# Performance work log

Hardware: AMD Instinct MI355X
Metric: run time of the kernel (lower is better)

## Reference

```python
import jax, jax.numpy as jnp
import numpy as np

DIM = 1024
HEADS = 16
HEAD_DIM = DIM // HEADS
WINDOW = 128


def setup_inputs() -> dict:
    key = jax.random.key(0)
    k1, k2, k3, k4 = jax.random.split(key, 4)
    B, T = 2, 2048
    x = jax.random.normal(k1, (B, T, DIM), dtype=jnp.float32)
    # nn.Linear(dim, 3*dim, bias=False): weight [3*dim, dim]; y = x @ W.T
    W_qkv = jax.random.normal(k2, (3 * DIM, DIM), dtype=jnp.float32) * (1.0 / np.sqrt(DIM))
    W_proj = jax.random.normal(k3, (DIM, DIM), dtype=jnp.float32) * (1.0 / np.sqrt(DIM))
    b_proj = jax.random.normal(k4, (DIM,), dtype=jnp.float32) * 0.01
    return {"x": x, "W_qkv": W_qkv, "W_proj": W_proj, "b_proj": b_proj}


def reference(x, W_qkv, W_proj, b_proj) -> jnp.ndarray:
    B, T, C = x.shape
    scale = HEAD_DIM ** -0.5
    qkv = jnp.einsum('btc,oc->bto', x, W_qkv)  # [B,T,3*D]
    qkv = qkv.reshape(B, T, 3, HEADS, HEAD_DIM)
    qkv = jnp.transpose(qkv, (2, 0, 3, 1, 4))  # [3,B,H,T,hd]
    q, k, v = qkv[0], qkv[1], qkv[2]
    # sliding-window mask: attend iff |i-j| <= WINDOW
    idx = jnp.arange(T)
    mask = jnp.abs(idx[:, None] - idx[None, :]) <= WINDOW  # [T,T]
    scores = jnp.einsum('bhqd,bhkd->bhqk', q, k) * scale  # [B,H,T,T]
    scores = jnp.where(mask[None, None], scores, jnp.finfo(scores.dtype).min)
    attn = jax.nn.softmax(scores, axis=-1)
    out = jnp.einsum('bhqk,bhkd->bhqd', attn, v)  # [B,H,T,hd]
    out = jnp.transpose(out, (0, 2, 1, 3)).reshape(B, T, C)
    return jnp.einsum('btc,oc->bto', out, W_proj) + b_proj
```

## Files before the change

### kernel.cpp

```cpp
#include <hip/hip_runtime.h>
#include <hip/hip_bf16.h>
#include <cstdint>
#include <cstddef>

#define DIMC 1024
#define HEADS 16
#define HD 64
#define WINDOW 128
#define BB 2
#define TT 2048
#define NTOK (BB*TT)
#define QKVN (3*DIMC)

typedef __bf16 bf16;
typedef __bf16 bf16x8 __attribute__((ext_vector_type(8)));
typedef __bf16 bf16x4 __attribute__((ext_vector_type(4)));
typedef float f32x4 __attribute__((ext_vector_type(4)));
typedef unsigned int u32;

typedef const __attribute__((address_space(1))) u32* gp1_t;
typedef __attribute__((address_space(3))) u32* lp3_t;

__device__ __forceinline__ void gload16(const void* g, void* l) {
  __builtin_amdgcn_global_load_lds((gp1_t)g, (lp3_t)l, 16, 0, 0);
}

__device__ __forceinline__ u32 lds_u32(const void* p) {
  return (u32)(uintptr_t)(__attribute__((address_space(3))) const void*)p;
}

__device__ __forceinline__ void BAR() {
  asm volatile("" ::: "memory");
  __builtin_amdgcn_s_barrier();
  asm volatile("" ::: "memory");
}

__global__ void cast3_kernel(const float* __restrict__ x,
                             const float* __restrict__ wq,
                             const float* __restrict__ wp,
                             bf16* __restrict__ xo,
                             bf16* __restrict__ wqo,
                             bf16* __restrict__ wpo) {
  const int NX = NTOK * DIMC / 4;
  const int NQ = QKVN * DIMC / 4;
  const int NP = DIMC * DIMC / 4;
  const int total = NX + NQ + NP;
  typedef float float4v __attribute__((ext_vector_type(4)));
  for (int i = blockIdx.x * blockDim.x + threadIdx.x; i < total;
       i += gridDim.x * blockDim.x) {
    const float4v* src; bf16* dst; int j;
    if (i < NX)            { src = (const float4v*)x;  dst = xo;  j = i; }
    else if (i < NX + NQ)  { src = (const float4v*)wq; dst = wqo; j = i - NX; }
    else                   { src = (const float4v*)wp; dst = wpo; j = i - NX - NQ; }
    float4v v = src[j];
    bf16x4 o;
    o[0] = (bf16)v[0]; o[1] = (bf16)v[1]; o[2] = (bf16)v[2]; o[3] = (bf16)v[3];
    ((bf16x4*)dst)[j] = o;
  }
}

__device__ __forceinline__ bf16x8 lds_frag(const bf16* base, int row, int colb) {
  const char* p = (const char*)base + row * 128 + (colb ^ ((row & 7) << 4));
  return *(const bf16x8*)p;
}

template<int N_, bool BF16OUT>
__global__ __launch_bounds__(256, 2) void gemm128_kernel(
    const bf16* __restrict__ A, const bf16* __restrict__ Bw,
    bf16* __restrict__ Cb, float* __restrict__ Cf,
    const float* __restrict__ bias) {
  constexpr int K = 1024;
  constexpr int NT = K / 64;
  __shared__ bf16 Al[2][128 * 64];
  __shared__ bf16 Bl[2][128 * 64];

  const int tid = threadIdx.x;
  const int w = tid >> 6, l = tid & 63;
  const int wm = w >> 1, wn = w & 1;
  const int lr = l & 15, lg = l >> 4;

  const int nwg = gridDim.x;
  const int bid = blockIdx.x;
  const int wg = (bid & 7) * (nwg >> 3) + (bid >> 3);
  const int bm = wg & 31;
  const int bn = wg >> 5;

  const char* Ag = (const char*)A + (size_t)(bm * 128) * 2048;
  const char* Bg = (const char*)Bw + (size_t)(bn * 128) * 2048;

  auto stageT = [&](bf16* lds, const char* gbase, int kt) {
#pragma unroll
    for (int i = 0; i < 4; i++) {
      const int R0 = w * 32 + i * 8;
      const int r = R0 + (l >> 3);
      const char* src = gbase + (size_t)r * 2048 + kt * 128
                        + (((l & 7) * 16) ^ ((r & 7) << 4));
      gload16(src, lds + R0 * 64);
    }
  };

  stageT(Al[0], Ag, 0); stageT(Bl[0], Bg, 0);
  stageT(Al[1], Ag, 1); stageT(Bl[1], Bg, 1);
  asm volatile("s_waitcnt vmcnt(8)" ::: "memory");
  BAR();

  f32x4 acc[4][4] = {};

  for (int kt = 0; kt < NT; ++kt) {
    const bf16* Ac = Al[kt & 1];
    const bf16* Bc = Bl[kt & 1];

    bf16x8 af[4][2], bf[4][2];
#pragma unroll
    for (int m = 0; m < 4; m++)
#pragma unroll
      for (int kk = 0; kk < 2; kk++)
        af[m][kk] = lds_frag(Ac, wm * 64 + m * 16 + lr, kk * 64 + lg * 16);
#pragma unroll
    for (int n = 0; n < 4; n++)
#pragma unroll
      for (int kk = 0; kk < 2; kk++)
        bf[n][kk] = lds_frag(Bc, wn * 64 + n * 16 + lr, kk * 64 + lg * 16);

    asm volatile("s_waitcnt lgkmcnt(0)" ::: "memory");
    __builtin_amdgcn_sched_barrier(0);
    BAR();

    if (kt + 2 < NT) {
      stageT(Al[kt & 1], Ag, kt + 2);
      stageT(Bl[kt & 1], Bg, kt + 2);
    }

    __builtin_amdgcn_s_setprio(1);
#pragma unroll
    for (int kk = 0; kk < 2; kk++)
#pragma unroll
      for (int m = 0; m < 4; m++)
#pragma unroll
        for (int n = 0; n < 4; n++)
          acc[m][n] = __builtin_amdgcn_mfma_f32_16x16x32_bf16(
              af[m][kk], bf[n][kk], acc[m][n], 0, 0, 0);
    __builtin_amdgcn_s_setprio(0);

    if (kt < NT - 2) asm volatile("s_waitcnt vmcnt(8)" ::: "memory");
    else             asm volatile("s_waitcnt vmcnt(0)" ::: "memory");
    BAR();
  }

#pragma unroll
  for (int m = 0; m < 4; m++) {
    const int row = bm * 128 + wm * 64 + m * 16 + lg * 4;
#pragma unroll
    for (int n = 0; n < 4; n++) {
      const int col = bn * 128 + wn * 64 + n * 16 + lr;
#pragma unroll
      for (int j = 0; j < 4; j++) {
        if constexpr (BF16OUT)
          Cb[(size_t)(row + j) * N_ + col] = (bf16)acc[m][n][j];
        else
          Cf[(size_t)(row + j) * N_ + col] = acc[m][n][j] + bias[col];
      }
    }
  }
}

__global__ __launch_bounds__(256, 4) void attn_kernel(const bf16* __restrict__ qkv,
                                                      bf16* __restrict__ out) {
  __shared__ bf16 Kl[2][64 * 64];
  __shared__ bf16 Vl[2][64 * 64];

  const int tid = threadIdx.x, w = tid >> 6, l = tid & 63;
  const int qb = blockIdx.x & 31, bh = blockIdx.x >> 5;
  const int b = bh >> 4, h = bh & 15;
  const int q0 = qb * 64;
  const int lr = l & 15, lg = l >> 4;
  const float SC = 0.18033688011f;

  const char* qkv_b = (const char*)qkv + (size_t)(b * TT) * (QKVN * 2);

  size_t koff[2]; u32 kdst[2];
#pragma unroll
  for (int i = 0; i < 2; i++) {
    const int R0 = 8 * (w + 4 * i);
    const int r = R0 + (l >> 3);
    const int colb = (((l & 7) * 16) ^ (((l >> 3) & 7) << 4));
    koff[i] = (size_t)r * (QKVN * 2) + (DIMC + h * HD) * 2 + colb;
    kdst[i] = (u32)(R0 * 64);
  }
  size_t voff[2]; u32 vdst[2];
#pragma unroll
  for (int i = 0; i < 2; i++) {
    const int c = tid + 256 * i;
    const int t = c >> 3, w_ = c & 7;
    const int kv = (t & 15) * 4 + (w_ >> 1);
    const int d  = (t >> 4) * 16 + (w_ & 1) * 8;
    voff[i] = (size_t)kv * (QKVN * 2) + (2 * DIMC + h * HD + d) * 2;
    vdst[i] = (u32)((w + 4 * i) * 512);
  }

  auto stage = [&](int buf, int kb) {
    const char* rowb = qkv_b + (size_t)(kb * 64) * (QKVN * 2);
#pragma unroll
    for (int i = 0; i < 2; i++)
      gload16(rowb + koff[i], &Kl[buf][kdst[i]]);
#pragma unroll
    for (int i = 0; i < 2; i++)
      gload16(rowb + voff[i], &Vl[buf][vdst[i]]);
  };

  bf16x8 qf[2];
  {
    const bf16* qp = qkv + (size_t)(b * TT + q0 + w * 16 + lr) * QKVN + h * HD + lg * 8;
    qf[0] = *(const bf16x8*)qp;
    qf[1] = *(const bf16x8*)(qp + 32);
  }

  f32x4 Oa[4] = {};
  float mrow = -1e30f, lrow = 0.f;

  int kb0 = qb - 2; if (kb0 < 0) kb0 = 0;
  int kb1 = qb + 2; if (kb1 > 31) kb1 = 31;

  stage(0, kb0);
  asm volatile("s_waitcnt vmcnt(0)" ::: "memory");
  BAR();

  for (int kb = kb0; kb <= kb1; ++kb) {
    const int c = (kb - kb0) & 1;
    if (kb + 1 <= kb1) stage(c ^ 1, kb + 1);

    const bf16* Kb = &Kl[c][0];
    f32x4 Sa[4] = {};
#pragma unroll
    for (int kf = 0; kf < 2; kf++)
#pragma unroll
      for (int nf = 0; nf < 4; nf++) {
        const char* kp = (const char*)Kb + (nf * 16 + lr) * 128
                         + ((kf * 64 + lg * 16) ^ ((lr & 7) << 4));
        bf16x8 kfr = *(const bf16x8*)kp;
        Sa[nf] = __builtin_amdgcn_mfma_f32_16x16x32_bf16(kfr, qf[kf], Sa[nf], 0, 0, 0);
      }

    bf16x4 tr0[4][2], tr1[4][2];
    {
      const u32 vbase = lds_u32(&Vl[c][0]) + l * 8;
#pragma unroll
      for (int nf = 0; nf < 4; nf++)
#pragma unroll
        for (int kf = 0; kf < 2; kf++) {
          const u32 a = vbase + (u32)((nf * 16 + kf * 8) * 128);
          asm volatile("ds_read_b64_tr_b16 %0, %1"
                       : "=v"(tr0[nf][kf]) : "v"(a));
          asm volatile("ds_read_b64_tr_b16 %0, %1 offset:512"
                       : "=v"(tr1[nf][kf]) : "v"(a));
        }
    }

    const int qrow = q0 + w * 16 + lr;
    const int kvb = kb * 64;
    float p[4][4];
    float mblk = -1e30f;
#pragma unroll
    for (int nf = 0; nf < 4; nf++)
#pragma unroll
      for (int j = 0; j < 4; j++) {
        int kv = kvb + nf * 16 + lg * 4 + j;
        int dq = qrow - kv;
        float s = Sa[nf][j] * SC;
        if (dq > WINDOW || dq < -WINDOW) s = -1e30f;
        p[nf][j] = s;
        mblk = fmaxf(mblk, s);
      }
    mblk = fmaxf(mblk, __shfl_xor(mblk, 16));
    mblk = fmaxf(mblk, __shfl_xor(mblk, 32));

    float mn = fmaxf(mrow, mblk);
    float scl = exp2f(mrow - mn);
    mrow = mn;

    float rsum = 0.f;
#pragma unroll
    for (int nf = 0; nf < 4; nf++)
#pragma unroll
      for (int j = 0; j < 4; j++) {
        float e = exp2f(p[nf][j] - mn);
        p[nf][j] = e;
        rsum += e;
      }
    rsum += __shfl_xor(rsum, 16);
    rsum += __shfl_xor(rsum, 32);
    lrow = lrow * scl + rsum;

    bf16x8 pa[2];
#pragma unroll
    for (int kf = 0; kf < 2; kf++)
#pragma unroll
      for (int e = 0; e < 4; e++) {
        pa[kf][e]     = (bf16)p[2 * kf][e];
        pa[kf][e + 4] = (bf16)p[2 * kf + 1][e];
      }

#pragma unroll
    for (int j = 0; j < 4; j++) {
      float so = __shfl(scl, lg * 4 + j);
#pragma unroll
      for (int nf = 0; nf < 4; nf++) Oa[nf][j] *= so;
    }

    asm volatile("s_waitcnt lgkmcnt(0)" ::: "memory");
    __builtin_amdgcn_sched_barrier(0);
#pragma unroll
    for (int nf = 0; nf < 4; nf++)
#pragma unroll
      for (int kf = 0; kf < 2; kf++) {
        bf16x8 vb;
#pragma unroll
        for (int e = 0; e < 4; e++) {
          vb[e]     = tr0[nf][kf][e];
          vb[e + 4] = tr1[nf][kf][e];
        }
        Oa[nf] = __builtin_amdgcn_mfma_f32_16x16x32_bf16(pa[kf], vb, Oa[nf], 0, 0, 0);
      }

    asm volatile("s_waitcnt vmcnt(0)" ::: "memory");
    BAR();
  }

  float lo[4];
#pragma unroll
  for (int j = 0; j < 4; j++) lo[j] = __shfl(lrow, lg * 4 + j);
#pragma unroll
  for (int nf = 0; nf < 4; nf++) {
#pragma unroll
    for (int j = 0; j < 4; j++) {
      int q = q0 + w * 16 + lg * 4 + j;
      int d = nf * 16 + lr;
      out[(size_t)(b * TT + q) * DIMC + h * HD + d] = (bf16)(Oa[nf][j] / lo[j]);
    }
  }
}

extern "C" void kernel_launch(void* const* d_in, const int* in_sizes, int n_in,
                              void* d_out, int out_size, void* d_ws, size_t ws_size,
                              hipStream_t stream) {
  const float* x     = (const float*)d_in[0];
  const float* Wqkv  = (const float*)d_in[1];
  const float* Wproj = (const float*)d_in[2];
  const float* bproj = (const float*)d_in[3];
  float* out = (float*)d_out;

  char* ws = (char*)d_ws;
  bf16* xb   = (bf16*)(ws);
  bf16* wqb  = (bf16*)(ws + 8388608);
  bf16* wpb  = (bf16*)(ws + 14680064);
  bf16* qkvb = (bf16*)(ws + 16777216);
  bf16* aob  = (bf16*)(ws + 41943040);

  cast3_kernel<<<2048, 256, 0, stream>>>(x, Wqkv, Wproj, xb, wqb, wpb);
  gemm128_kernel<QKVN, true><<<768, 256, 0, stream>>>(xb, wqb, qkvb, nullptr, nullptr);
  attn_kernel<<<1024, 256, 0, stream>>>(qkvb, aob);
  gemm128_kernel<DIMC, false><<<256, 256, 0, stream>>>(aob, wpb, nullptr, out, bproj);
}
```

Measured before the change: 90.22 us.

## Narrow QKV GEMM tile, widen attention query block, triple-buffer KV

```diff
diff --git a/kernel.cpp b/kernel.cpp
--- a/kernel.cpp
+++ b/kernel.cpp
@@ -64,15 +64,16 @@
   return *(const bf16x8*)p;
 }
 
-template<int N_, bool BF16OUT>
-__global__ __launch_bounds__(256, 2) void gemm128_kernel(
+template<int BN, int N_, bool BF16OUT>
+__global__ __launch_bounds__(256, 2) void gemm_kernel(
     const bf16* __restrict__ A, const bf16* __restrict__ Bw,
     bf16* __restrict__ Cb, float* __restrict__ Cf,
     const float* __restrict__ bias) {
-  constexpr int K = 1024;
-  constexpr int NT = K / 64;
+  constexpr int NT = 16;
+  constexpr int NB = BN / 32;
+  constexpr int LPT = 4 + BN / 32;
   __shared__ bf16 Al[2][128 * 64];
-  __shared__ bf16 Bl[2][128 * 64];
+  __shared__ bf16 Bl[2][BN * 64];
 
   const int tid = threadIdx.x;
   const int w = tid >> 6, l = tid & 63;
@@ -86,49 +87,60 @@
   const int bn = wg >> 5;
 
   const char* Ag = (const char*)A + (size_t)(bm * 128) * 2048;
-  const char* Bg = (const char*)Bw + (size_t)(bn * 128) * 2048;
-
-  auto stageT = [&](bf16* lds, const char* gbase, int kt) {
+  const char* Bg = (const char*)Bw + (size_t)(bn * BN) * 2048;
+
+  auto stageA = [&](bf16* lds, int kt) {
 #pragma unroll
     for (int i = 0; i < 4; i++) {
       const int R0 = w * 32 + i * 8;
       const int r = R0 + (l >> 3);
-      const char* src = gbase + (size_t)r * 2048 + kt * 128
+      const char* src = Ag + (size_t)r * 2048 + kt * 128
                         + (((l & 7) * 16) ^ ((r & 7) << 4));
       gload16(src, lds + R0 * 64);
     }
   };
-
-  stageT(Al[0], Ag, 0); stageT(Bl[0], Bg, 0);
-  stageT(Al[1], Ag, 1); stageT(Bl[1], Bg, 1);
-  asm volatile("s_waitcnt vmcnt(8)" ::: "memory");
+  auto stageB = [&](bf16* lds, int kt) {
+#pragma unroll
+    for (int i = 0; i < NB; i++) {
+      const int R0 = w * (BN / 4) + i * 8;
+      const int r = R0 + (l >> 3);
+      const char* src = Bg + (size_t)r * 2048 + kt * 128
+                        + (((l & 7) * 16) ^ ((r & 7) << 4));
+      gload16(src, lds + R0 * 64);
+    }
+  };
+
+  stageA(Al[0], 0); stageB(Bl[0], 0);
+  stageA(Al[1], 1); stageB(Bl[1], 1);
+  if constexpr (LPT == 7) asm volatile("s_waitcnt vmcnt(7)" ::: "memory");
+  else                    asm volatile("s_waitcnt vmcnt(8)" ::: "memory");
   BAR();
 
-  f32x4 acc[4][4] = {};
+  f32x4 acc[4][NB] = {};
 
   for (int kt = 0; kt < NT; ++kt) {
     const bf16* Ac = Al[kt & 1];
     const bf16* Bc = Bl[kt & 1];
 
-    bf16x8 af[4][2], bf[4][2];
+    bf16x8 af[4][2], bf[NB][2];
 #pragma unroll
     for (int m = 0; m < 4; m++)
 #pragma unroll
       for (int kk = 0; kk < 2; kk++)
         af[m][kk] = lds_frag(Ac, wm * 64 + m * 16 + lr, kk * 64 + lg * 16);
 #pragma unroll
-    for (int n = 0; n < 4; n++)
+    for (int n = 0; n < NB; n++)
 #pragma unroll
       for (int kk = 0; kk < 2; kk++)
-        bf[n][kk] = lds_frag(Bc, wn * 64 + n * 16 + lr, kk * 64 + lg * 16);
+        bf[n][kk] = lds_frag(Bc, wn * (BN / 2) + n * 16 + lr, kk * 64 + lg * 16);
 
     asm volatile("s_waitcnt lgkmcnt(0)" ::: "memory");
     __builtin_amdgcn_sched_barrier(0);
     BAR();
 
     if (kt + 2 < NT) {
-      stageT(Al[kt & 1], Ag, kt + 2);
-      stageT(Bl[kt & 1], Bg, kt + 2);
+      stageA(Al[kt & 1], kt + 2);
+      stageB(Bl[kt & 1], kt + 2);
     }
 
     __builtin_amdgcn_s_setprio(1);
@@ -137,13 +149,17 @@
 #pragma unroll
       for (int m = 0; m < 4; m++)
 #pragma unroll
-        for (int n = 0; n < 4; n++)
+        for (int n = 0; n < NB; n++)
           acc[m][n] = __builtin_amdgcn_mfma_f32_16x16x32_bf16(
               af[m][kk], bf[n][kk], acc[m][n], 0, 0, 0);
     __builtin_amdgcn_s_setprio(0);
 
-    if (kt < NT - 2) asm volatile("s_waitcnt vmcnt(8)" ::: "memory");
-    else             asm volatile("s_waitcnt vmcnt(0)" ::: "memory");
+    if (kt < NT - 2) {
+      if constexpr (LPT == 7) asm volatile("s_waitcnt vmcnt(7)" ::: "memory");
+      else                    asm volatile("s_waitcnt vmcnt(8)" ::: "memory");
+    } else {
+      asm volatile("s_waitcnt vmcnt(0)" ::: "memory");
+    }
     BAR();
   }
 
@@ -151,8 +167,8 @@
   for (int m = 0; m < 4; m++) {
     const int row = bm * 128 + wm * 64 + m * 16 + lg * 4;
 #pragma unroll
-    for (int n = 0; n < 4; n++) {
-      const int col = bn * 128 + wn * 64 + n * 16 + lr;
+    for (int n = 0; n < NB; n++) {
+      const int col = bn * BN + wn * (BN / 2) + n * 16 + lr;
 #pragma unroll
       for (int j = 0; j < 4; j++) {
         if constexpr (BF16OUT)
@@ -164,15 +180,15 @@
   }
 }
 
-__global__ __launch_bounds__(256, 4) void attn_kernel(const bf16* __restrict__ qkv,
+__global__ __launch_bounds__(256, 2) void attn_kernel(const bf16* __restrict__ qkv,
                                                       bf16* __restrict__ out) {
-  __shared__ bf16 Kl[2][64 * 64];
-  __shared__ bf16 Vl[2][64 * 64];
+  __shared__ bf16 Kl[3][64 * 64];
+  __shared__ bf16 Vl[3][64 * 64];
 
   const int tid = threadIdx.x, w = tid >> 6, l = tid & 63;
-  const int qb = blockIdx.x & 31, bh = blockIdx.x >> 5;
+  const int qb = blockIdx.x & 15, bh = blockIdx.x >> 4;
   const int b = bh >> 4, h = bh & 15;
-  const int q0 = qb * 64;
+  const int q0 = qb * 128;
   const int lr = l & 15, lg = l >> 4;
   const float SC = 0.18033688011f;
 
@@ -208,29 +224,32 @@
       gload16(rowb + voff[i], &Vl[buf][vdst[i]]);
   };
 
-  bf16x8 qf[2];
-  {
-    const bf16* qp = qkv + (size_t)(b * TT + q0 + w * 16 + lr) * QKVN + h * HD + lg * 8;
-    qf[0] = *(const bf16x8*)qp;
-    qf[1] = *(const bf16x8*)(qp + 32);
-  }
-
-  f32x4 Oa[4] = {};
-  float mrow = -1e30f, lrow = 0.f;
-
-  int kb0 = qb - 2; if (kb0 < 0) kb0 = 0;
-  int kb1 = qb + 2; if (kb1 > 31) kb1 = 31;
+  bf16x8 qf[2][2];
+#pragma unroll
+  for (int qi = 0; qi < 2; qi++) {
+    const bf16* qp = qkv + (size_t)(b * TT + q0 + w * 32 + qi * 16 + lr) * QKVN
+                     + h * HD + lg * 8;
+    qf[qi][0] = *(const bf16x8*)qp;
+    qf[qi][1] = *(const bf16x8*)(qp + 32);
+  }
+
+  f32x4 Oa[2][4] = {};
+  float mrow[2] = {-1e30f, -1e30f}, lrow[2] = {0.f, 0.f};
+
+  int kb0 = 2 * qb - 2; if (kb0 < 0) kb0 = 0;
+  int kb1 = 2 * qb + 3; if (kb1 > 31) kb1 = 31;
 
   stage(0, kb0);
-  asm volatile("s_waitcnt vmcnt(0)" ::: "memory");
+  stage(1, kb0 + 1);
+  asm volatile("s_waitcnt vmcnt(4)" ::: "memory");
   BAR();
 
   for (int kb = kb0; kb <= kb1; ++kb) {
-    const int c = (kb - kb0) & 1;
-    if (kb + 1 <= kb1) stage(c ^ 1, kb + 1);
+    const int c = (kb - kb0) % 3;
+    if (kb + 2 <= kb1) stage((c + 2) % 3, kb + 2);
 
     const bf16* Kb = &Kl[c][0];
-    f32x4 Sa[4] = {};
+    f32x4 Sa[2][4] = {};
 #pragma unroll
     for (int kf = 0; kf < 2; kf++)
 #pragma unroll
@@ -238,7 +257,8 @@
         const char* kp = (const char*)Kb + (nf * 16 + lr) * 128
                          + ((kf * 64 + lg * 16) ^ ((lr & 7) << 4));
         bf16x8 kfr = *(const bf16x8*)kp;
-        Sa[nf] = __builtin_amdgcn_mfma_f32_16x16x32_bf16(kfr, qf[kf], Sa[nf], 0, 0, 0);
+        Sa[0][nf] = __builtin_amdgcn_mfma_f32_16x16x32_bf16(kfr, qf[0][kf], Sa[0][nf], 0, 0, 0);
+        Sa[1][nf] = __builtin_amdgcn_mfma_f32_16x16x32_bf16(kfr, qf[1][kf], Sa[1][nf], 0, 0, 0);
       }
 
     bf16x4 tr0[4][2], tr1[4][2];
@@ -256,55 +276,58 @@
         }
     }
 
-    const int qrow = q0 + w * 16 + lr;
     const int kvb = kb * 64;
-    float p[4][4];
-    float mblk = -1e30f;
-#pragma unroll
-    for (int nf = 0; nf < 4; nf++)
+    float scl[2];
+    bf16x8 pa[2][2];
+#pragma unroll
+    for (int qi = 0; qi < 2; qi++) {
+      const int qrow = q0 + w * 32 + qi * 16 + lr;
+      float mblk = -1e30f;
+#pragma unroll
+      for (int nf = 0; nf < 4; nf++)
+#pragma unroll
+        for (int j = 0; j < 4; j++) {
+          int kv = kvb + nf * 16 + lg * 4 + j;
+          int dq = qrow - kv;
+          float s = Sa[qi][nf][j] * SC;
+          if (dq > WINDOW || dq < -WINDOW) s = -1e30f;
+          Sa[qi][nf][j] = s;
+          mblk = fmaxf(mblk, s);
+        }
+      mblk = fmaxf(mblk, __shfl_xor(mblk, 16));
+      mblk = fmaxf(mblk, __shfl_xor(mblk, 32));
+
+      float mn = fmaxf(mrow[qi], mblk);
+      scl[qi] = exp2f(mrow[qi] - mn);
+      mrow[qi] = mn;
+
+      float rsum = 0.f;
+#pragma unroll
+      for (int nf = 0; nf < 4; nf++)
+#pragma unroll
+        for (int j = 0; j < 4; j++) {
+          float e = exp2f(Sa[qi][nf][j] - mn);
+          Sa[qi][nf][j] = e;
+          rsum += e;
+        }
+      rsum += __shfl_xor(rsum, 16);
+      rsum += __shfl_xor(rsum, 32);
+      lrow[qi] = lrow[qi] * scl[qi] + rsum;
+
+#pragma unroll
+      for (int kf = 0; kf < 2; kf++)
+#pragma unroll
+        for (int e = 0; e < 4; e++) {
+          pa[qi][kf][e]     = (bf16)Sa[qi][2 * kf][e];
+          pa[qi][kf][e + 4] = (bf16)Sa[qi][2 * kf + 1][e];
+        }
+
 #pragma unroll
       for (int j = 0; j < 4; j++) {
-        int kv = kvb + nf * 16 + lg * 4 + j;
-        int dq = qrow - kv;
-        float s = Sa[nf][j] * SC;
-        if (dq > WINDOW || dq < -WINDOW) s = -1e30f;
-        p[nf][j] = s;
-        mblk = fmaxf(mblk, s);
-      }
-    mblk = fmaxf(mblk, __shfl_xor(mblk, 16));
-    mblk = fmaxf(mblk, __shfl_xor(mblk, 32));
-
-    float mn = fmaxf(mrow, mblk);
-    float scl = exp2f(mrow - mn);
-    mrow = mn;
-
-    float rsum = 0.f;
-#pragma unroll
-    for (int nf = 0; nf < 4; nf++)
-#pragma unroll
-      for (int j = 0; j < 4; j++) {
-        float e = exp2f(p[nf][j] - mn);
-        p[nf][j] = e;
-        rsum += e;
-      }
-    rsum += __shfl_xor(rsum, 16);
-    rsum += __shfl_xor(rsum, 32);
-    lrow = lrow * scl + rsum;
-
-    bf16x8 pa[2];
-#pragma unroll
-    for (int kf = 0; kf < 2; kf++)
-#pragma unroll
-      for (int e = 0; e < 4; e++) {
-        pa[kf][e]     = (bf16)p[2 * kf][e];
-        pa[kf][e + 4] = (bf16)p[2 * kf + 1][e];
-      }
-
-#pragma unroll
-    for (int j = 0; j < 4; j++) {
-      float so = __shfl(scl, lg * 4 + j);
-#pragma unroll
-      for (int nf = 0; nf < 4; nf++) Oa[nf][j] *= so;
+        float so = __shfl(scl[qi], lg * 4 + j);
+#pragma unroll
+        for (int nf = 0; nf < 4; nf++) Oa[qi][nf][j] *= so;
+      }
     }
 
     asm volatile("s_waitcnt lgkmcnt(0)" ::: "memory");
@@ -319,23 +342,30 @@
           vb[e]     = tr0[nf][kf][e];
           vb[e + 4] = tr1[nf][kf][e];
         }
-        Oa[nf] = __builtin_amdgcn_mfma_f32_16x16x32_bf16(pa[kf], vb, Oa[nf], 0, 0, 0);
-      }
-
-    asm volatile("s_waitcnt vmcnt(0)" ::: "memory");
+        Oa[0][nf] = __builtin_amdgcn_mfma_f32_16x16x32_bf16(pa[0][kf], vb, Oa[0][nf], 0, 0, 0);
+        Oa[1][nf] = __builtin_amdgcn_mfma_f32_16x16x32_bf16(pa[1][kf], vb, Oa[1][nf], 0, 0, 0);
+      }
+
+    if (kb < kb1) {
+      if (kb + 2 <= kb1) asm volatile("s_waitcnt vmcnt(4)" ::: "memory");
+      else               asm volatile("s_waitcnt vmcnt(0)" ::: "memory");
+    }
     BAR();
   }
 
-  float lo[4];
-#pragma unroll
-  for (int j = 0; j < 4; j++) lo[j] = __shfl(lrow, lg * 4 + j);
-#pragma unroll
-  for (int nf = 0; nf < 4; nf++) {
-#pragma unroll
-    for (int j = 0; j < 4; j++) {
-      int q = q0 + w * 16 + lg * 4 + j;
-      int d = nf * 16 + lr;
-      out[(size_t)(b * TT + q) * DIMC + h * HD + d] = (bf16)(Oa[nf][j] / lo[j]);
+#pragma unroll
+  for (int qi = 0; qi < 2; qi++) {
+    float lo[4];
+#pragma unroll
+    for (int j = 0; j < 4; j++) lo[j] = __shfl(lrow[qi], lg * 4 + j);
+#pragma unroll
+    for (int nf = 0; nf < 4; nf++) {
+#pragma unroll
+      for (int j = 0; j < 4; j++) {
+        int q = q0 + w * 32 + qi * 16 + lg * 4 + j;
+        int d = nf * 16 + lr;
+        out[(size_t)(b * TT + q) * DIMC + h * HD + d] = (bf16)(Oa[qi][nf][j] / lo[j]);
+      }
     }
   }
 }
@@ -357,7 +387,7 @@
   bf16* aob  = (bf16*)(ws + 41943040);
 
   cast3_kernel<<<2048, 256, 0, stream>>>(x, Wqkv, Wproj, xb, wqb, wpb);
-  gemm128_kernel<QKVN, true><<<768, 256, 0, stream>>>(xb, wqb, qkvb, nullptr, nullptr);
-  attn_kernel<<<1024, 256, 0, stream>>>(qkvb, aob);
-  gemm128_kernel<DIMC, false><<<256, 256, 0, stream>>>(aob, wpb, nullptr, out, bproj);
-}
+  gemm_kernel<96, QKVN, true><<<1024, 256, 0, stream>>>(xb, wqb, qkvb, nullptr, nullptr);
+  attn_kernel<<<512, 256, 0, stream>>>(qkvb, aob);
+  gemm_kernel<128, DIMC, false><<<256, 256, 0, stream>>>(aob, wpb, nullptr, out, bproj);
+}
```

Result: no change. 90.04 us (-0.2%).

## Use 512-thread blocks for GEMM and attention, triple-buffer KV, lazy rescale

Applied to the files above, without the earlier changes.

```diff
diff --git a/kernel.cpp b/kernel.cpp
--- a/kernel.cpp
+++ b/kernel.cpp
@@ -65,33 +65,32 @@
 }
 
 template<int N_, bool BF16OUT>
-__global__ __launch_bounds__(256, 2) void gemm128_kernel(
+__global__ __launch_bounds__(512, 4) void gemm_kernel(
     const bf16* __restrict__ A, const bf16* __restrict__ Bw,
     bf16* __restrict__ Cb, float* __restrict__ Cf,
     const float* __restrict__ bias) {
-  constexpr int K = 1024;
-  constexpr int NT = K / 64;
+  constexpr int NT = 16;
+  constexpr int Nb = N_ / 128;
   __shared__ bf16 Al[2][128 * 64];
   __shared__ bf16 Bl[2][128 * 64];
 
   const int tid = threadIdx.x;
   const int w = tid >> 6, l = tid & 63;
-  const int wm = w >> 1, wn = w & 1;
+  const int wm = w >> 2, wn = w & 3;
   const int lr = l & 15, lg = l >> 4;
 
-  const int nwg = gridDim.x;
   const int bid = blockIdx.x;
-  const int wg = (bid & 7) * (nwg >> 3) + (bid >> 3);
-  const int bm = wg & 31;
-  const int bn = wg >> 5;
+  const int x = bid & 7, i = bid >> 3;
+  const int bm = 8 * (x >> 1) + (i & 7);
+  const int bn = (Nb / 2) * (x & 1) + (i >> 3);
 
   const char* Ag = (const char*)A + (size_t)(bm * 128) * 2048;
   const char* Bg = (const char*)Bw + (size_t)(bn * 128) * 2048;
 
   auto stageT = [&](bf16* lds, const char* gbase, int kt) {
 #pragma unroll
-    for (int i = 0; i < 4; i++) {
-      const int R0 = w * 32 + i * 8;
+    for (int i2 = 0; i2 < 2; i2++) {
+      const int R0 = w * 16 + i2 * 8;
       const int r = R0 + (l >> 3);
       const char* src = gbase + (size_t)r * 2048 + kt * 128
                         + (((l & 7) * 16) ^ ((r & 7) << 4));
@@ -101,26 +100,26 @@
 
   stageT(Al[0], Ag, 0); stageT(Bl[0], Bg, 0);
   stageT(Al[1], Ag, 1); stageT(Bl[1], Bg, 1);
-  asm volatile("s_waitcnt vmcnt(8)" ::: "memory");
+  asm volatile("s_waitcnt vmcnt(4)" ::: "memory");
   BAR();
 
-  f32x4 acc[4][4] = {};
+  f32x4 acc[4][2] = {};
 
   for (int kt = 0; kt < NT; ++kt) {
     const bf16* Ac = Al[kt & 1];
     const bf16* Bc = Bl[kt & 1];
 
-    bf16x8 af[4][2], bf[4][2];
+    bf16x8 af[4][2], bf[2][2];
 #pragma unroll
     for (int m = 0; m < 4; m++)
 #pragma unroll
       for (int kk = 0; kk < 2; kk++)
         af[m][kk] = lds_frag(Ac, wm * 64 + m * 16 + lr, kk * 64 + lg * 16);
 #pragma unroll
-    for (int n = 0; n < 4; n++)
+    for (int n = 0; n < 2; n++)
 #pragma unroll
       for (int kk = 0; kk < 2; kk++)
-        bf[n][kk] = lds_frag(Bc, wn * 64 + n * 16 + lr, kk * 64 + lg * 16);
+        bf[n][kk] = lds_frag(Bc, wn * 32 + n * 16 + lr, kk * 64 + lg * 16);
 
     asm volatile("s_waitcnt lgkmcnt(0)" ::: "memory");
     __builtin_amdgcn_sched_barrier(0);
@@ -137,12 +136,12 @@
 #pragma unroll
       for (int m = 0; m < 4; m++)
 #pragma unroll
-        for (int n = 0; n < 4; n++)
+        for (int n = 0; n < 2; n++)
           acc[m][n] = __builtin_amdgcn_mfma_f32_16x16x32_bf16(
               af[m][kk], bf[n][kk], acc[m][n], 0, 0, 0);
     __builtin_amdgcn_s_setprio(0);
 
-    if (kt < NT - 2) asm volatile("s_waitcnt vmcnt(8)" ::: "memory");
+    if (kt < NT - 2) asm volatile("s_waitcnt vmcnt(4)" ::: "memory");
     else             asm volatile("s_waitcnt vmcnt(0)" ::: "memory");
     BAR();
   }
@@ -151,8 +150,8 @@
   for (int m = 0; m < 4; m++) {
     const int row = bm * 128 + wm * 64 + m * 16 + lg * 4;
 #pragma unroll
-    for (int n = 0; n < 4; n++) {
-      const int col = bn * 128 + wn * 64 + n * 16 + lr;
+    for (int n = 0; n < 2; n++) {
+      const int col = bn * 128 + wn * 32 + n * 16 + lr;
 #pragma unroll
       for (int j = 0; j < 4; j++) {
         if constexpr (BF16OUT)
@@ -164,48 +163,42 @@
   }
 }
 
-__global__ __launch_bounds__(256, 4) void attn_kernel(const bf16* __restrict__ qkv,
+__global__ __launch_bounds__(512, 4) void attn_kernel(const bf16* __restrict__ qkv,
                                                       bf16* __restrict__ out) {
-  __shared__ bf16 Kl[2][64 * 64];
-  __shared__ bf16 Vl[2][64 * 64];
+  __shared__ bf16 Kl[3][64 * 64];
+  __shared__ bf16 Vl[3][64 * 64];
 
   const int tid = threadIdx.x, w = tid >> 6, l = tid & 63;
-  const int qb = blockIdx.x & 31, bh = blockIdx.x >> 5;
+  const int qb = blockIdx.x & 15, bh = blockIdx.x >> 4;
   const int b = bh >> 4, h = bh & 15;
-  const int q0 = qb * 64;
+  const int q0 = qb * 128;
   const int lr = l & 15, lg = l >> 4;
   const float SC = 0.18033688011f;
 
   const char* qkv_b = (const char*)qkv + (size_t)(b * TT) * (QKVN * 2);
 
-  size_t koff[2]; u32 kdst[2];
-#pragma unroll
-  for (int i = 0; i < 2; i++) {
-    const int R0 = 8 * (w + 4 * i);
+  size_t koff; u32 kdst;
+  {
+    const int R0 = 8 * w;
     const int r = R0 + (l >> 3);
     const int colb = (((l & 7) * 16) ^ (((l >> 3) & 7) << 4));
-    koff[i] = (size_t)r * (QKVN * 2) + (DIMC + h * HD) * 2 + colb;
-    kdst[i] = (u32)(R0 * 64);
-  }
-  size_t voff[2]; u32 vdst[2];
-#pragma unroll
-  for (int i = 0; i < 2; i++) {
-    const int c = tid + 256 * i;
+    koff = (size_t)r * (QKVN * 2) + (DIMC + h * HD) * 2 + colb;
+    kdst = (u32)(R0 * 64);
+  }
+  size_t voff; u32 vdst;
+  {
+    const int c = tid;
     const int t = c >> 3, w_ = c & 7;
     const int kv = (t & 15) * 4 + (w_ >> 1);
     const int d  = (t >> 4) * 16 + (w_ & 1) * 8;
-    voff[i] = (size_t)kv * (QKVN * 2) + (2 * DIMC + h * HD + d) * 2;
-    vdst[i] = (u32)((w + 4 * i) * 512);
+    voff = (size_t)kv * (QKVN * 2) + (2 * DIMC + h * HD + d) * 2;
+    vdst = (u32)(w * 512);
   }
 
   auto stage = [&](int buf, int kb) {
     const char* rowb = qkv_b + (size_t)(kb * 64) * (QKVN * 2);
-#pragma unroll
-    for (int i = 0; i < 2; i++)
-      gload16(rowb + koff[i], &Kl[buf][kdst[i]]);
-#pragma unroll
-    for (int i = 0; i < 2; i++)
-      gload16(rowb + voff[i], &Vl[buf][vdst[i]]);
+    gload16(rowb + koff, &Kl[buf][kdst]);
+    gload16(rowb + voff, &Vl[buf][vdst]);
   };
 
   bf16x8 qf[2];
@@ -218,16 +211,17 @@
   f32x4 Oa[4] = {};
   float mrow = -1e30f, lrow = 0.f;
 
-  int kb0 = qb - 2; if (kb0 < 0) kb0 = 0;
-  int kb1 = qb + 2; if (kb1 > 31) kb1 = 31;
+  int kb0 = 2 * qb - 2; if (kb0 < 0) kb0 = 0;
+  int kb1 = 2 * qb + 3; if (kb1 > 31) kb1 = 31;
 
   stage(0, kb0);
-  asm volatile("s_waitcnt vmcnt(0)" ::: "memory");
+  stage(1, kb0 + 1);
+  asm volatile("s_waitcnt vmcnt(2)" ::: "memory");
   BAR();
 
   for (int kb = kb0; kb <= kb1; ++kb) {
-    const int c = (kb - kb0) & 1;
-    if (kb + 1 <= kb1) stage(c ^ 1, kb + 1);
+    const int c = (kb - kb0) % 3;
+    if (kb + 2 <= kb1) stage((c + 2) % 3, kb + 2);
 
     const bf16* Kb = &Kl[c][0];
     f32x4 Sa[4] = {};
@@ -256,9 +250,8 @@
         }
     }
 
+    const int kvb = kb * 64;
     const int qrow = q0 + w * 16 + lr;
-    const int kvb = kb * 64;
-    float p[4][4];
     float mblk = -1e30f;
 #pragma unroll
     for (int nf = 0; nf < 4; nf++)
@@ -268,44 +261,46 @@
         int dq = qrow - kv;
         float s = Sa[nf][j] * SC;
         if (dq > WINDOW || dq < -WINDOW) s = -1e30f;
-        p[nf][j] = s;
+        Sa[nf][j] = s;
         mblk = fmaxf(mblk, s);
       }
     mblk = fmaxf(mblk, __shfl_xor(mblk, 16));
     mblk = fmaxf(mblk, __shfl_xor(mblk, 32));
 
-    float mn = fmaxf(mrow, mblk);
-    float scl = exp2f(mrow - mn);
-    mrow = mn;
+    if (!__all(mblk <= mrow + 8.f)) {
+      float mn = fmaxf(mrow, mblk);
+      float sc = exp2f(mrow - mn);
+      mrow = mn;
+      lrow *= sc;
+#pragma unroll
+      for (int j = 0; j < 4; j++) {
+        float so = __shfl(sc, lg * 4 + j);
+#pragma unroll
+        for (int nf = 0; nf < 4; nf++) Oa[nf][j] *= so;
+      }
+    }
 
     float rsum = 0.f;
 #pragma unroll
     for (int nf = 0; nf < 4; nf++)
 #pragma unroll
       for (int j = 0; j < 4; j++) {
-        float e = exp2f(p[nf][j] - mn);
-        p[nf][j] = e;
+        float e = exp2f(Sa[nf][j] - mrow);
+        Sa[nf][j] = e;
         rsum += e;
       }
     rsum += __shfl_xor(rsum, 16);
     rsum += __shfl_xor(rsum, 32);
-    lrow = lrow * scl + rsum;
+    lrow += rsum;
 
     bf16x8 pa[2];
 #pragma unroll
     for (int kf = 0; kf < 2; kf++)
 #pragma unroll
       for (int e = 0; e < 4; e++) {
-        pa[kf][e]     = (bf16)p[2 * kf][e];
-        pa[kf][e + 4] = (bf16)p[2 * kf + 1][e];
-      }
-
-#pragma unroll
-    for (int j = 0; j < 4; j++) {
-      float so = __shfl(scl, lg * 4 + j);
-#pragma unroll
-      for (int nf = 0; nf < 4; nf++) Oa[nf][j] *= so;
-    }
+        pa[kf][e]     = (bf16)Sa[2 * kf][e];
+        pa[kf][e + 4] = (bf16)Sa[2 * kf + 1][e];
+      }
 
     asm volatile("s_waitcnt lgkmcnt(0)" ::: "memory");
     __builtin_amdgcn_sched_barrier(0);
@@ -322,7 +317,10 @@
         Oa[nf] = __builtin_amdgcn_mfma_f32_16x16x32_bf16(pa[kf], vb, Oa[nf], 0, 0, 0);
       }
 
-    asm volatile("s_waitcnt vmcnt(0)" ::: "memory");
+    if (kb < kb1) {
+      if (kb + 2 <= kb1) asm volatile("s_waitcnt vmcnt(2)" ::: "memory");
+      else               asm volatile("s_waitcnt vmcnt(0)" ::: "memory");
+    }
     BAR();
   }
 
@@ -357,7 +355,7 @@
   bf16* aob  = (bf16*)(ws + 41943040);
 
   cast3_kernel<<<2048, 256, 0, stream>>>(x, Wqkv, Wproj, xb, wqb, wpb);
-  gemm128_kernel<QKVN, true><<<768, 256, 0, stream>>>(xb, wqb, qkvb, nullptr, nullptr);
-  attn_kernel<<<1024, 256, 0, stream>>>(qkvb, aob);
-  gemm128_kernel<DIMC, false><<<256, 256, 0, stream>>>(aob, wpb, nullptr, out, bproj);
-}
+  gemm_kernel<QKVN, true><<<768, 512, 0, stream>>>(xb, wqb, qkvb, nullptr, nullptr);
+  attn_kernel<<<512, 512, 0, stream>>>(qkvb, aob);
+  gemm_kernel<DIMC, false><<<256, 512, 0, stream>>>(aob, wpb, nullptr, out, bproj);
+}
```

After: 81.18 us. -10.0%, faster.
